# Kernel optimization log

Hardware: AMD Instinct MI355X
Metric: run time of the kernel (lower is better)

## Reference

```python
import jax, jax.numpy as jnp
import numpy as np

DIM = 1024
NUM_HEADS = 16
HEAD_DIM = DIM // NUM_HEADS
SCALE = HEAD_DIM ** -0.5


def setup_inputs() -> dict:
    key = jax.random.key(0)
    ks = jax.random.split(key, 5)
    B, N = 2, 2048
    x = jax.random.normal(ks[0], (B, N, DIM), dtype=jnp.float32)
    # nn.Linear weights: stored as [out, in]; we keep that convention.
    w_qkv = jax.random.normal(ks[1], (3 * DIM, DIM), dtype=jnp.float32) * (DIM ** -0.5)
    b_qkv = jax.random.normal(ks[2], (3 * DIM,), dtype=jnp.float32) * 0.02
    w_proj = jax.random.normal(ks[3], (DIM, DIM), dtype=jnp.float32) * (DIM ** -0.5)
    b_proj = jax.random.normal(ks[4], (DIM,), dtype=jnp.float32) * 0.02
    return {"x": x, "w_qkv": w_qkv, "b_qkv": b_qkv, "w_proj": w_proj, "b_proj": b_proj}


def reference(x, w_qkv, b_qkv, w_proj, b_proj):
    B, N, C = x.shape
    H, D = NUM_HEADS, HEAD_DIM
    qkv = x @ w_qkv.T + b_qkv                      # [B, N, 3C]
    qkv = qkv.reshape(B, N, 3, H, D)
    q = qkv[:, :, 0].transpose(0, 2, 1, 3)         # [B, H, N, D]
    k = qkv[:, :, 1].transpose(0, 2, 1, 3)
    v = qkv[:, :, 2].transpose(0, 2, 1, 3)
    attn = jnp.einsum("bhnd,bhmd->bhnm", q, k) * SCALE  # [B, H, N, N]
    attn = jax.nn.softmax(attn, axis=-1)
    out = jnp.einsum("bhnm,bhmd->bhnd", attn, v)   # [B, H, N, D]
    out = out.transpose(0, 2, 1, 3).reshape(B, N, C)
    return out @ w_proj.T + b_proj
```

## Files before the change

kernel.cpp:

```cpp
#include <hip/hip_runtime.h>
#include <math.h>

#define DIMC   1024
#define NHEADS 16
#define HDIM   64
#define BATCH  2
#define SEQ    2048

#define MTOT   (BATCH * SEQ)
#define QKVN   (3 * DIMC)
#define QKVSZ  ((size_t)BATCH * NHEADS * SEQ * HDIM)
#define HEADEL ((size_t)SEQ * HDIM)

#define QSCALE 0.18033688011112042f

typedef __attribute__((ext_vector_type(8))) short bf16x8;
typedef __attribute__((ext_vector_type(4))) short bf16x4;
typedef __attribute__((ext_vector_type(4))) float f32x4;

static __device__ inline short f2bf(float f) {
    union { float f; unsigned u; } v; v.f = f;
    unsigned r = v.u + 0x7fffu + ((v.u >> 16) & 1u);
    return (short)(r >> 16);
}
static __device__ inline short f2bf_fast(float f) {
    union { float f; unsigned u; } v; v.f = f;
    return (short)((v.u + 0x8000u) >> 16);
}

#if __has_builtin(__builtin_amdgcn_exp2f)
#define EXP2F(x) __builtin_amdgcn_exp2f(x)
#else
#define EXP2F(x) exp2f(x)
#endif

#define NXB  (MTOT * DIMC / 2048)
#define NWQB (QKVN * DIMC / 2048)
#define NWPB (DIMC * DIMC / 2048)

__global__ __launch_bounds__(256) void cast_all(
    const float* __restrict__ x,  const float* __restrict__ wq,
    const float* __restrict__ wp, short* __restrict__ xb,
    short* __restrict__ wqb, short* __restrict__ wpb)
{
    const float* in; short* out; int base;
    int bid = blockIdx.x;
    if (bid < NXB)              { in = x;  out = xb;  base = bid; }
    else if (bid < NXB + NWQB)  { in = wq; out = wqb; base = bid - NXB; }
    else                        { in = wp; out = wpb; base = bid - NXB - NWQB; }
    int i = (base * 256 + threadIdx.x) * 8;
    float4 a = *(const float4*)&in[i];
    float4 b = *(const float4*)&in[i + 4];
    bf16x8 o;
    o[0] = f2bf(a.x); o[1] = f2bf(a.y); o[2] = f2bf(a.z); o[3] = f2bf(a.w);
    o[4] = f2bf(b.x); o[5] = f2bf(b.y); o[6] = f2bf(b.z); o[7] = f2bf(b.w);
    *(bf16x8*)&out[i] = o;
}

__device__ __forceinline__ void gload16(const void* g, void* l) {
    __builtin_amdgcn_global_load_lds(
        (const __attribute__((address_space(1))) unsigned*)g,
        (__attribute__((address_space(3))) unsigned*)l, 16, 0, 0);
}

#define BAR() do { __builtin_amdgcn_s_barrier(); \
                   __builtin_amdgcn_sched_barrier(0); } while (0)
#define VWAIT8() asm volatile("s_waitcnt vmcnt(8)" ::: "memory")
#define VWAIT0() asm volatile("s_waitcnt vmcnt(0)" ::: "memory")

__device__ __forceinline__ void stage_panel(const short* __restrict__ src,
                                            int row0, int k0,
                                            short* dst, int tid)
{
#pragma unroll
    for (int u = 0; u < 2; ++u) {
        const int gidx = u * 512 + tid;
        const int rl   = gidx >> 3;
        const int cc   = gidx & 7;
        gload16(&src[(size_t)(row0 + rl) * 1024 + k0 + ((cc ^ (rl & 7)) << 3)],
                &dst[(size_t)gidx << 3]);
    }
}

template<int MH, int NH>
__device__ __forceinline__ void phase_compute(
    const short* As, const short* Bs,
    int wm, int wn, int lid, int quad, f32x4 (&acc)[8][4])
{
    bf16x8 af[4][2], bfr[2][2];
#pragma unroll
    for (int i2 = 0; i2 < 4; ++i2) {
        const int r = wm + (MH * 4 + i2) * 16 + lid;
#pragma unroll
        for (int kk = 0; kk < 2; ++kk)
            af[i2][kk] = *(const bf16x8*)
                &As[r * 64 + (((kk * 4 + quad) ^ (r & 7)) << 3)];
    }
#pragma unroll
    for (int j2 = 0; j2 < 2; ++j2) {
        const int rb = wn + (NH * 2 + j2) * 16 + lid;
#pragma unroll
        for (int kk = 0; kk < 2; ++kk)
            bfr[j2][kk] = *(const bf16x8*)
                &Bs[rb * 64 + (((kk * 4 + quad) ^ (rb & 7)) << 3)];
    }
    __builtin_amdgcn_s_setprio(1);
#pragma unroll
    for (int i2 = 0; i2 < 4; ++i2)
#pragma unroll
        for (int j2 = 0; j2 < 2; ++j2)
#pragma unroll
            for (int kk = 0; kk < 2; ++kk)
                acc[MH * 4 + i2][NH * 2 + j2] =
                    __builtin_amdgcn_mfma_f32_16x16x32_bf16(
                        af[i2][kk], bfr[j2][kk],
                        acc[MH * 4 + i2][NH * 2 + j2], 0, 0, 0);
    __builtin_amdgcn_s_setprio(0);
}

__global__ __launch_bounds__(512, 2) void qkv_mfma(
    const short* __restrict__ xb,
    const short* __restrict__ wb,
    const float* __restrict__ bias,
    short* __restrict__ qkvb)
{
    extern __shared__ short lds[];

    const int tid = threadIdx.x;
    const int T  = (blockIdx.x & 7) * 24 + (blockIdx.x >> 3);
    const int m0 = (T / 12) * 256;
    const int j0 = (T % 12) * 256;

    const int lane = tid & 63;
    const int w    = tid >> 6;
    const int quad = lane >> 4;
    const int lid  = lane & 15;
    const int wm = (w >> 2) * 128;
    const int wn = (w & 3) * 64;

    f32x4 acc[8][4];
#pragma unroll
    for (int i = 0; i < 8; ++i)
#pragma unroll
        for (int j = 0; j < 4; ++j) acc[i][j] = (f32x4){0.f, 0.f, 0.f, 0.f};

    stage_panel(xb, m0,       0, lds,                 tid);
    stage_panel(xb, m0 + 128, 0, lds + 8192,          tid);
    stage_panel(wb, j0,       0, lds + 32768,         tid);
    stage_panel(wb, j0 + 128, 0, lds + 32768 + 8192,  tid);

#pragma unroll 2
    for (int kt = 0; kt < 15; ++kt) {
        const int cb = (kt & 1) << 14;
        const int nb = (~kt & 1) << 14;
        const int k1 = (kt + 1) << 6;
        const short* Ac = lds + cb;
        const short* Bc = lds + 32768 + cb;
        short* An = lds + nb;
        short* Bn = lds + 32768 + nb;

        stage_panel(xb, m0,       k1, An,        tid);
        stage_panel(xb, m0 + 128, k1, An + 8192, tid);
        stage_panel(wb, j0,       k1, Bn,        tid);
        stage_panel(wb, j0 + 128, k1, Bn + 8192, tid);

        VWAIT8(); BAR();
        phase_compute<0, 0>(Ac, Bc, wm, wn, lid, quad, acc);
        BAR();
        phase_compute<0, 1>(Ac, Bc, wm, wn, lid, quad, acc);
        BAR();
        phase_compute<1, 0>(Ac, Bc, wm, wn, lid, quad, acc);
        BAR();
        phase_compute<1, 1>(Ac, Bc, wm, wn, lid, quad, acc);
        BAR();
    }
    {
        const short* Ac = lds + 16384;
        const short* Bc = lds + 32768 + 16384;
        VWAIT0(); BAR();
        phase_compute<0, 0>(Ac, Bc, wm, wn, lid, quad, acc);
        BAR();
        phase_compute<0, 1>(Ac, Bc, wm, wn, lid, quad, acc);
        BAR();
        phase_compute<1, 0>(Ac, Bc, wm, wn, lid, quad, acc);
        BAR();
        phase_compute<1, 1>(Ac, Bc, wm, wn, lid, quad, acc);
    }

    const int s = j0 >> 10;

    if (s == 0) {
#pragma unroll
        for (int jb = 0; jb < 4; ++jb) {
            const int jj = j0 + wn + jb * 16 + lid;
            const int hh = (jj & 1023) >> 6;
            const int dd = jj & 63;
            const float bv = bias[jj];
#pragma unroll
            for (int i = 0; i < 8; ++i)
#pragma unroll
                for (int r = 0; r < 4; ++r) {
                    const int mrow = m0 + wm + i * 16 + quad * 4 + r;
                    const int b_ = mrow >> 11, nn = mrow & 2047;
                    qkvb[((size_t)(b_ * NHEADS + hh) * SEQ + nn) * HDIM + dd] =
                        f2bf((acc[i][jb][r] + bv) * QSCALE);
                }
        }
    } else if (s == 1) {
#pragma unroll
        for (int jb = 0; jb < 4; ++jb) {
            const int jj = j0 + wn + jb * 16 + lid;
            const int hh = (jj & 1023) >> 6;
            const int dd = jj & 63;
            const int c2 = dd >> 5;
            const int qd = (dd >> 3) & 3;
            const int jo = dd & 7;
            const float bv = bias[jj];
#pragma unroll
            for (int i = 0; i < 8; ++i) {
                const int mrow0 = m0 + wm + i * 16;
                const int b_ = mrow0 >> 11;
                const int n0 = mrow0 & 2047;
                const int t32 = n0 >> 5;
                const int i16 = (n0 >> 4) & 1;
                const int c = quad & 1;
                const int lidb = (i16 * 2 + (quad >> 1)) * 4;
                size_t base = QKVSZ + (size_t)(b_ * NHEADS + hh) * HEADEL +
                              (size_t)(t32 * 4 + c2 * 2 + c) * 512 +
                              (qd * 16 + lidb) * 8 + jo;
#pragma unroll
                for (int r = 0; r < 4; ++r)
                    qkvb[base + r * 8] = f2bf(acc[i][jb][r] + bv);
            }
        }
    } else {
#pragma unroll
        for (int jb = 0; jb < 4; ++jb) {
            const int jj = j0 + wn + jb * 16 + lid;
            const int hh = (jj & 1023) >> 6;
            const int dd = jj & 63;
            const int fb = dd >> 4;
            const int dl = dd & 15;
            const float bv = bias[jj];
#pragma unroll
            for (int i = 0; i < 8; ++i) {
                const int mrow0 = m0 + wm + i * 16 + quad * 4;
                const int b_ = mrow0 >> 11, n0 = mrow0 & 2047;
                const int t32 = n0 >> 5;
                const int i16 = (n0 >> 4) & 1;
                const int quadpp = i16 * 2 + (quad >> 1);
                bf16x4 o;
#pragma unroll
                for (int r = 0; r < 4; ++r) o[r] = f2bf(acc[i][jb][r] + bv);
                *(bf16x4*)&qkvb[2 * QKVSZ + (size_t)(b_ * NHEADS + hh) * HEADEL +
                                (size_t)(t32 * 4 + fb) * 512 +
                                (quadpp * 16 + dl) * 8 + (quad & 1) * 4] = o;
            }
        }
    }
}

__global__ __launch_bounds__(256, 2) void attn_mfma(
    const short* __restrict__ qkvb,
    short* __restrict__ aob)
{
    __shared__ float Osm[2][4][4][4][64];
    __shared__ float Lsm[3][64];

    const int tid  = threadIdx.x;
    const int sp   = tid >> 6;
    const int lane = tid & 63;
    const int quad = lane >> 4;
    const int lid  = lane & 15;

    const int qbase = blockIdx.x * 64;
    const int h  = blockIdx.y;
    const int b  = blockIdx.z;

    const short* Qh = qkvb + (size_t)(b * NHEADS + h) * HEADEL;
    const short* Kf = Qh + QKVSZ;
    const short* Vf = qkvb + 2 * QKVSZ + (size_t)(b * NHEADS + h) * HEADEL;

    bf16x8 bQ[4][2];
#pragma unroll
    for (int g = 0; g < 4; ++g)
#pragma unroll
        for (int c = 0; c < 2; ++c)
            bQ[g][c] = *(const bf16x8*)&Qh[(size_t)(qbase + g * 16 + lid) * HDIM +
                                           c * 32 + quad * 8];

    f32x4 O[4][4];
    f32x4 L[4];
#pragma unroll
    for (int g = 0; g < 4; ++g) {
        L[g] = (f32x4){0.f, 0.f, 0.f, 0.f};
#pragma unroll
        for (int fb = 0; fb < 4; ++fb) O[g][fb] = (f32x4){0.f, 0.f, 0.f, 0.f};
    }
    const bf16x8 ones8 = {(short)0x3F80, (short)0x3F80, (short)0x3F80, (short)0x3F80,
                          (short)0x3F80, (short)0x3F80, (short)0x3F80, (short)0x3F80};

#pragma unroll 2
    for (int cc = 0; cc < SEQ / 128; ++cc) {
        const int t = sp * (SEQ / 128) + cc;
        bf16x8 aK[2][2];
#pragma unroll
        for (int c = 0; c < 2; ++c)
#pragma unroll
            for (int c2 = 0; c2 < 2; ++c2)
                aK[c][c2] = *(const bf16x8*)&Kf[(size_t)(t * 4 + c2 * 2 + c) * 512 +
                                                lane * 8];
        bf16x8 aV[4];
#pragma unroll
        for (int fb = 0; fb < 4; ++fb)
            aV[fb] = *(const bf16x8*)&Vf[(size_t)(t * 4 + fb) * 512 + lane * 8];

#pragma unroll
        for (int g = 0; g < 4; ++g) {
            f32x4 s0 = (f32x4){0.f, 0.f, 0.f, 0.f};
            f32x4 s1 = (f32x4){0.f, 0.f, 0.f, 0.f};
            s0 = __builtin_amdgcn_mfma_f32_16x16x32_bf16(aK[0][0], bQ[g][0], s0, 0, 0, 0);
            s1 = __builtin_amdgcn_mfma_f32_16x16x32_bf16(aK[1][0], bQ[g][0], s1, 0, 0, 0);
            s0 = __builtin_amdgcn_mfma_f32_16x16x32_bf16(aK[0][1], bQ[g][1], s0, 0, 0, 0);
            s1 = __builtin_amdgcn_mfma_f32_16x16x32_bf16(aK[1][1], bQ[g][1], s1, 0, 0, 0);
            bf16x8 P;
#pragma unroll
            for (int r = 0; r < 4; ++r) {
                P[r]     = f2bf_fast(EXP2F(s0[r]));
                P[4 + r] = f2bf_fast(EXP2F(s1[r]));
            }
            L[g] = __builtin_amdgcn_mfma_f32_16x16x32_bf16(ones8, P, L[g], 0, 0, 0);
#pragma unroll
            for (int fb = 0; fb < 4; ++fb)
                O[g][fb] = __builtin_amdgcn_mfma_f32_16x16x32_bf16(
                    aV[fb], P, O[g][fb], 0, 0, 0);
        }
    }

    if (sp != 0 && quad == 0)
#pragma unroll
        for (int g = 0; g < 4; ++g) Lsm[sp - 1][g * 16 + lid] = L[g][0];

    if (sp == 1 || sp == 3) {
        const int buf = sp >> 1;
#pragma unroll
        for (int g = 0; g < 4; ++g)
#pragma unroll
            for (int fb = 0; fb < 4; ++fb)
#pragma unroll
                for (int r = 0; r < 4; ++r)
                    Osm[buf][g][fb][r][lane] = O[g][fb][r];
    }
    __syncthreads();
    if (sp == 0 || sp == 2) {
        const int buf = sp >> 1;
#pragma unroll
        for (int g = 0; g < 4; ++g)
#pragma unroll
            for (int fb = 0; fb < 4; ++fb)
#pragma unroll
                for (int r = 0; r < 4; ++r)
                    O[g][fb][r] += Osm[buf][g][fb][r][lane];
    }
    __syncthreads();
    if (sp == 2) {
#pragma unroll
        for (int g = 0; g < 4; ++g)
#pragma unroll
            for (int fb = 0; fb < 4; ++fb)
#pragma unroll
                for (int r = 0; r < 4; ++r)
                    Osm[0][g][fb][r][lane] = O[g][fb][r];
    }
    __syncthreads();
    if (sp == 0) {
#pragma unroll
        for (int g = 0; g < 4; ++g) {
            const float lt = L[g][0] + Lsm[0][g * 16 + lid] +
                             Lsm[1][g * 16 + lid] + Lsm[2][g * 16 + lid];
            const float inv = 1.f / lt;
            const int n = qbase + g * 16 + lid;
            size_t base = ((size_t)(b * SEQ + n)) * DIMC + h * HDIM;
#pragma unroll
            for (int fb = 0; fb < 4; ++fb) {
                bf16x4 o;
#pragma unroll
                for (int r = 0; r < 4; ++r)
                    o[r] = f2bf((O[g][fb][r] + Osm[0][g][fb][r][lane]) * inv);
                *(bf16x4*)&aob[base + fb * 16 + quad * 4] = o;
            }
        }
    }
}

__global__ __launch_bounds__(256, 2) void proj_mfma(
    const short* __restrict__ ab,
    const short* __restrict__ wb,
    const float* __restrict__ bias,
    float* __restrict__ out)
{
    __shared__ __attribute__((aligned(16))) short Asm[2 * 64 * 32];
    __shared__ __attribute__((aligned(16))) short Bsm[2 * 128 * 32];

    const int tid = threadIdx.x;
    const int m0 = blockIdx.y * 64;
    const int j0 = blockIdx.x * 128;

    const int lane = tid & 63;
    const int w    = tid >> 6;
    const int quad = lane >> 4;
    const int lid  = lane & 15;
    const int wm = (w >> 1) * 32, wn = (w & 1) * 64;

    const int srow = lane >> 2;
    const int skc  = (lane & 3) * 8;

    f32x4 acc[2][4];
#pragma unroll
    for (int i = 0; i < 2; ++i)
#pragma unroll
        for (int j = 0; j < 4; ++j) acc[i][j] = (f32x4){0.f, 0.f, 0.f, 0.f};

    for (int k0 = 0; k0 < 1024; k0 += 64) {
        __syncthreads();
#pragma unroll
        for (int u = 0; u < 2; ++u) {
            const int combo = w * 2 + u;
            const int hh = combo >> 2, rb = combo & 3;
            const int row = rb * 16 + srow;
            gload16(&ab[(size_t)(m0 + row) * 1024 + k0 + hh * 32 + skc],
                    &Asm[hh * 2048 + row * 32 + skc]);
        }
#pragma unroll
        for (int u = 0; u < 4; ++u) {
            const int combo = w * 4 + u;
            const int hh = combo >> 3, rb = combo & 7;
            const int row = rb * 16 + srow;
            gload16(&wb[(size_t)(j0 + row) * 1024 + k0 + hh * 32 + skc],
                    &Bsm[hh * 4096 + row * 32 + skc]);
        }
        __syncthreads();

#pragma unroll
        for (int hh = 0; hh < 2; ++hh) {
            bf16x8 af[2], bfr[4];
#pragma unroll
            for (int i = 0; i < 2; ++i)
                af[i] = *(const bf16x8*)&Asm[hh * 2048 + (wm + i * 16 + lid) * 32 + quad * 8];
#pragma unroll
            for (int j = 0; j < 4; ++j)
                bfr[j] = *(const bf16x8*)&Bsm[hh * 4096 + (wn + j * 16 + lid) * 32 + quad * 8];
#pragma unroll
            for (int i = 0; i < 2; ++i)
#pragma unroll
                for (int j = 0; j < 4; ++j)
                    acc[i][j] = __builtin_amdgcn_mfma_f32_16x16x32_bf16(
                        af[i], bfr[j], acc[i][j], 0, 0, 0);
        }
    }

#pragma unroll
    for (int jb = 0; jb < 4; ++jb) {
        const int jj = j0 + wn + jb * 16 + lid;
        const float bv = bias[jj];
#pragma unroll
        for (int i = 0; i < 2; ++i)
#pragma unroll
            for (int r = 0; r < 4; ++r) {
                const int mrow = m0 + wm + i * 16 + quad * 4 + r;
                out[(size_t)mrow * DIMC + jj] = acc[i][jb][r] + bv;
            }
    }
}

extern "C" void kernel_launch(void* const* d_in, const int* in_sizes, int n_in,
                              void* d_out, int out_size, void* d_ws, size_t ws_size,
                              hipStream_t stream) {
    const float* x      = (const float*)d_in[0];
    const float* w_qkv  = (const float*)d_in[1];
    const float* b_qkv  = (const float*)d_in[2];
    const float* w_proj = (const float*)d_in[3];
    const float* b_proj = (const float*)d_in[4];
    float* out = (float*)d_out;

    short* qkvb   = (short*)d_ws;
    short* xb     = qkvb + 3 * QKVSZ;
    short* wqkvb  = xb + (size_t)MTOT * DIMC;
    short* wprojb = wqkvb + (size_t)QKVN * DIMC;
    short* aob    = wprojb + (size_t)DIMC * DIMC;

    hipFuncSetAttribute((const void*)qkv_mfma,
                        hipFuncAttributeMaxDynamicSharedMemorySize, 131072);

    cast_all<<<NXB + NWQB + NWPB, 256, 0, stream>>>(x, w_qkv, w_proj,
                                                    xb, wqkvb, wprojb);

    qkv_mfma<<<192, 512, 131072, stream>>>(xb, wqkvb, b_qkv, qkvb);

    dim3 g2(SEQ / 64, NHEADS, BATCH);
    attn_mfma<<<g2, 256, 0, stream>>>(qkvb, aob);

    dim3 g3(DIMC / 128, MTOT / 64);
    proj_mfma<<<g3, 256, 0, stream>>>(aob, wprojb, b_proj, out);
}
```

Measured before the change: 181.6 us.

## Remap attention blocks per XCD, use packed bf16 convert and MFMA priority hints

The attention grid becomes a flat 1D launch, and block ids are remapped so that all query blocks of a given (batch, head) pair land on the same XCD. This is meant to improve L2 reuse of that head's K/V. The scalar bf16 rounding of the softmax probabilities is replaced with the packed v_cvt_pk_bf16_f32 instruction, which halves the conversion instruction count. s_setprio is raised around the MFMA groups so that waves issuing matrix ops get priority over waves doing exp work. The remap assumes blocks are assigned round-robin to the 8 XCDs, and the conversion now rounds to nearest-even instead of the fast add-and-shift.

```diff
diff --git a/kernel.cpp b/kernel.cpp
--- a/kernel.cpp
+++ b/kernel.cpp
@@ -23,9 +23,11 @@
     unsigned r = v.u + 0x7fffu + ((v.u >> 16) & 1u);
     return (short)(r >> 16);
 }
-static __device__ inline short f2bf_fast(float f) {
-    union { float f; unsigned u; } v; v.f = f;
-    return (short)((v.u + 0x8000u) >> 16);
+
+static __device__ inline unsigned cvt_pk_bf16(float lo, float hi) {
+    unsigned r;
+    asm("v_cvt_pk_bf16_f32 %0, %1, %2" : "=v"(r) : "v"(lo), "v"(hi));
+    return r;
 }
 
 #if __has_builtin(__builtin_amdgcn_exp2f)
@@ -273,9 +275,14 @@
     const int quad = lane >> 4;
     const int lid  = lane & 15;
 
-    const int qbase = blockIdx.x * 64;
-    const int h  = blockIdx.y;
-    const int b  = blockIdx.z;
+    const int bid  = blockIdx.x;
+    const int xcd  = bid & 7;
+    const int slot = bid >> 3;
+    const int pair = xcd * 4 + (slot >> 5);
+    const int qblk = slot & 31;
+    const int h = pair & 15;
+    const int b = pair >> 4;
+    const int qbase = qblk * 64;
 
     const short* Qh = qkvb + (size_t)(b * NHEADS + h) * HEADEL;
     const short* Kf = Qh + QKVSZ;
@@ -319,21 +326,24 @@
         for (int g = 0; g < 4; ++g) {
             f32x4 s0 = (f32x4){0.f, 0.f, 0.f, 0.f};
             f32x4 s1 = (f32x4){0.f, 0.f, 0.f, 0.f};
+            __builtin_amdgcn_s_setprio(1);
             s0 = __builtin_amdgcn_mfma_f32_16x16x32_bf16(aK[0][0], bQ[g][0], s0, 0, 0, 0);
             s1 = __builtin_amdgcn_mfma_f32_16x16x32_bf16(aK[1][0], bQ[g][0], s1, 0, 0, 0);
             s0 = __builtin_amdgcn_mfma_f32_16x16x32_bf16(aK[0][1], bQ[g][1], s0, 0, 0, 0);
             s1 = __builtin_amdgcn_mfma_f32_16x16x32_bf16(aK[1][1], bQ[g][1], s1, 0, 0, 0);
-            bf16x8 P;
-#pragma unroll
-            for (int r = 0; r < 4; ++r) {
-                P[r]     = f2bf_fast(EXP2F(s0[r]));
-                P[4 + r] = f2bf_fast(EXP2F(s1[r]));
-            }
-            L[g] = __builtin_amdgcn_mfma_f32_16x16x32_bf16(ones8, P, L[g], 0, 0, 0);
+            __builtin_amdgcn_s_setprio(0);
+            union { unsigned u[4]; bf16x8 v; } P;
+            P.u[0] = cvt_pk_bf16(EXP2F(s0[0]), EXP2F(s0[1]));
+            P.u[1] = cvt_pk_bf16(EXP2F(s0[2]), EXP2F(s0[3]));
+            P.u[2] = cvt_pk_bf16(EXP2F(s1[0]), EXP2F(s1[1]));
+            P.u[3] = cvt_pk_bf16(EXP2F(s1[2]), EXP2F(s1[3]));
+            __builtin_amdgcn_s_setprio(1);
+            L[g] = __builtin_amdgcn_mfma_f32_16x16x32_bf16(ones8, P.v, L[g], 0, 0, 0);
 #pragma unroll
             for (int fb = 0; fb < 4; ++fb)
                 O[g][fb] = __builtin_amdgcn_mfma_f32_16x16x32_bf16(
-                    aV[fb], P, O[g][fb], 0, 0, 0);
+                    aV[fb], P.v, O[g][fb], 0, 0, 0);
+            __builtin_amdgcn_s_setprio(0);
         }
     }
 
@@ -497,8 +507,7 @@
 
     qkv_mfma<<<192, 512, 131072, stream>>>(xb, wqkvb, b_qkv, qkvb);
 
-    dim3 g2(SEQ / 64, NHEADS, BATCH);
-    attn_mfma<<<g2, 256, 0, stream>>>(qkvb, aob);
+    attn_mfma<<<BATCH * NHEADS * (SEQ / 64), 256, 0, stream>>>(qkvb, aob);
 
     dim3 g3(DIMC / 128, MTOT / 64);
     proj_mfma<<<g3, 256, 0, stream>>>(aob, wprojb, b_proj, out);
```

Result: faster. 177.0 us (-2.6%).
